# Optimization experiments

Hardware: AMD Instinct MI355X
Metric: run time of the kernel (lower is better)

## Reference

```python
import jax, jax.numpy as jnp
import numpy as np

D, H, KVH, HD = 2048, 16, 8, 128
D1, D2 = 32, 64  # get_decompose_dim(2048)
BITS = 8


def fake_quant(x, bits=BITS):
    # per-row (last-axis) symmetric fake quant with straight-through estimator
    qmax = float(2 ** (bits - 1) - 1)
    s = jnp.maximum(jnp.max(jnp.abs(x), axis=-1, keepdims=True) / qmax, 1e-8)
    q = jnp.clip(jnp.round(x / s), -qmax, qmax) * s
    return x + jax.lax.stop_gradient(q - x)


def rotate_half(x):
    h = x.shape[-1] // 2
    return jnp.concatenate([-x[..., h:], x[..., :h]], axis=-1)


def setup_inputs() -> dict:
    key = jax.random.key(0)
    ks = jax.random.split(key, 10)
    B, S = 1, 2048
    hidden_states = jax.random.normal(ks[0], (B, S, D), jnp.float32)
    # rotary embeddings
    inv_freq = 1.0 / (10000.0 ** (jnp.arange(0, HD, 2, dtype=jnp.float32) / HD))
    t = jnp.arange(S, dtype=jnp.float32)
    freqs = t[:, None] * inv_freq[None, :]
    emb = jnp.concatenate([freqs, freqs], axis=-1)
    cos, sin = jnp.cos(emb)[None], jnp.sin(emb)[None]  # [1,S,HD]
    # projection weights
    Wq = jax.random.normal(ks[1], (H * HD, D), jnp.float32) * 0.02
    Wk = jax.random.normal(ks[2], (KVH * HD, D), jnp.float32) * 0.02
    Wv = jax.random.normal(ks[3], (KVH * HD, D), jnp.float32) * 0.02
    Wo = jax.random.normal(ks[4], (D, H * HD), jnp.float32) * 0.02
    # learned invertible transforms (near-identity for conditioning)
    L = jnp.eye(D1) + 0.02 * jax.random.normal(ks[5], (D1, D1), jnp.float32)
    R = jnp.eye(D2) + 0.02 * jax.random.normal(ks[6], (D2, D2), jnp.float32)
    diag = 1.0 + 0.1 * jax.random.uniform(ks[7], (D,), jnp.float32)
    Tk = jnp.eye(HD) + 0.02 * jax.random.normal(ks[8], (HD, HD), jnp.float32)
    Tv = jnp.eye(HD) + 0.02 * jax.random.normal(ks[9], (HD, HD), jnp.float32)
    return dict(hidden_states=hidden_states, cos=cos, sin=sin, Wq=Wq, Wk=Wk,
                Wv=Wv, Wo=Wo, L=L, R=R, diag=diag, Tk=Tk, Tv=Tv)


def reference(hidden_states, cos, sin, Wq, Wk, Wv, Wo, L, R, diag, Tk, Tv):
    B, S, _ = hidden_states.shape
    groups = H // KVH
    scale = HD ** -0.5
    # ---- ln_trans: x' = (x * diag) @ kron(L, R) ----
    P = diag[:, None] * jnp.kron(L, R)               # [D, D]
    Pinv = jnp.kron(jnp.linalg.inv(L), jnp.linalg.inv(R)) * (1.0 / diag)[None, :]
    x = hidden_states @ P
    x_q = fake_quant(x)                               # per-token activation quant
    # ---- QKV with transform fused into weights (qa_trans), then weight quant ----
    q = x_q @ fake_quant(Wq @ Pinv.T).T               # [B,S,H*HD]
    k = x_q @ fake_quant(Wk @ Pinv.T).T               # [B,S,KVH*HD]
    Wv_eff = jnp.einsum('hd,khD->kdD', Tv, (Wv @ Pinv.T).reshape(KVH, HD, D))
    v = x_q @ fake_quant(Wv_eff.reshape(KVH * HD, D)).T  # v already in Tv space
    # ---- heads + RoPE ----
    q = q.reshape(B, S, H, HD).transpose(0, 2, 1, 3)
    k = k.reshape(B, S, KVH, HD).transpose(0, 2, 1, 3)
    v = v.reshape(B, S, KVH, HD).transpose(0, 2, 1, 3)
    c, s_ = cos[:, None], sin[:, None]                # [1,1,S,HD]
    q = q * c + rotate_half(q) * s_
    k = k * c + rotate_half(k) * s_
    # ---- kcache trans + quant: q @ inv(Tk)^T, k @ Tk (dot product preserved) ----
    q = q @ jnp.linalg.inv(Tk).T
    k = fake_quant(k @ Tk)
    v = fake_quant(v)
    # ---- eager causal attention with GQA ----
    k = jnp.repeat(k, groups, axis=1)
    v = jnp.repeat(v, groups, axis=1)
    scores = jnp.einsum('bhqd,bhkd->bhqk', q, k) * scale
    mask = jnp.tril(jnp.ones((S, S), bool))
    scores = jnp.where(mask, scores, jnp.finfo(scores.dtype).min)
    w = jax.nn.softmax(scores, axis=-1)
    o = jnp.einsum('bhqk,bhkd->bhqd', w, v)
    o = o.transpose(0, 2, 1, 3).reshape(B, S, H * HD)
    # ---- undo vcache trans per head, then quantized o_proj ----
    o = (o.reshape(B, S, H, HD) @ jnp.linalg.inv(Tv)).reshape(B, S, H * HD)
    out = fake_quant(o) @ fake_quant(Wo).T
    return out
```

## Files before the change

kernel.cpp:

```cpp
#include <hip/hip_runtime.h>
#include <math.h>

typedef unsigned short u16;
typedef __attribute__((ext_vector_type(8))) short bf16x8;
typedef __attribute__((ext_vector_type(4))) float f32x4;

__device__ __forceinline__ u16 f2bf(float x) {
    union { float f; unsigned int u; } c; c.f = x;
    unsigned int r = c.u + 0x7fffu + ((c.u >> 16) & 1u);
    return (u16)(r >> 16);
}
__device__ __forceinline__ float bf2f(u16 h) {
    union { unsigned int u; float f; } c; c.u = ((unsigned int)h) << 16;
    return c.f;
}
__device__ __forceinline__ bf16x8 ld16(const u16* p) {
    bf16x8 r;
    ((uint2*)&r)[0] = *(const uint2*)p;
    ((uint2*)&r)[1] = *(const uint2*)(p + 4);
    return r;
}
__device__ __forceinline__ void st8(u16* dst, uint4 r) {
    *(uint2*)dst = make_uint2(r.x, r.y);
    *(uint2*)(dst + 4) = make_uint2(r.z, r.w);
}
__device__ __forceinline__ void cvt8(const float4& v0, const float4& v1,
                                     uint4& hi, uint4& lo) {
    float vv[8] = {v0.x, v0.y, v0.z, v0.w, v1.x, v1.y, v1.z, v1.w};
    u16 h[8], l[8];
#pragma unroll
    for (int e = 0; e < 8; ++e) {
        h[e] = f2bf(vv[e]);
        l[e] = f2bf(vv[e] - bf2f(h[e]));
    }
    hi.x = h[0] | ((unsigned)h[1] << 16); hi.y = h[2] | ((unsigned)h[3] << 16);
    hi.z = h[4] | ((unsigned)h[5] << 16); hi.w = h[6] | ((unsigned)h[7] << 16);
    lo.x = l[0] | ((unsigned)l[1] << 16); lo.y = l[2] | ((unsigned)l[3] << 16);
    lo.z = l[4] | ((unsigned)l[5] << 16); lo.w = l[6] | ((unsigned)l[7] << 16);
}

__global__ __launch_bounds__(1024) void p0_kernel(
    const float* __restrict__ A0, float* __restrict__ I0,
    const float* __restrict__ A1, float* __restrict__ I1,
    const float* __restrict__ A2, float* __restrict__ I2,
    const float* __restrict__ A3, float* __restrict__ I3,
    const float* __restrict__ X, const float* __restrict__ dg,
    const float* __restrict__ Lk, const float* __restrict__ Rk,
    u16* __restrict__ Yq, float* __restrict__ Ysc) {
    const int tid = threadIdx.x;
    if (blockIdx.x < 4) {
        __shared__ float rowbuf[2][128];
        const float* A; float* out; int N;
        switch (blockIdx.x) {
            case 0:  A = A0; out = I0; N = 32;  break;
            case 1:  A = A1; out = I1; N = 64;  break;
            case 2:  A = A2; out = I2; N = 128; break;
            default: A = A3; out = I3; N = 128; break;
        }
        const int i = tid >> 3, g = tid & 7, c0 = g * 16;
        const int rl = (i & 7) << 3;
        float r[16];
#pragma unroll
        for (int e = 0; e < 16; ++e) {
            int j = c0 + e;
            r[e] = (i < N && j < N) ? A[i * N + j] : ((i == j) ? 1.0f : 0.0f);
        }
        if (i == 0) {
            float ip = 1.0f / __shfl(r[0], rl, 64);
#pragma unroll
            for (int e = 0; e < 16; ++e)
                rowbuf[0][c0 + e] = (c0 + e == 0) ? ip : r[e] * ip;
        }
        __syncthreads();
        const int ng = N >> 4;
        for (int k16 = 0; k16 < ng; ++k16) {
#pragma unroll
            for (int e = 0; e < 16; ++e) {
                const int k = (k16 << 4) + e;
                const int pb = k & 1;
                float ci = __shfl(r[e], rl + k16, 64);
                float4 rb0 = *(const float4*)&rowbuf[pb][c0];
                float4 rb1 = *(const float4*)&rowbuf[pb][c0 + 4];
                float4 rb2 = *(const float4*)&rowbuf[pb][c0 + 8];
                float4 rb3 = *(const float4*)&rowbuf[pb][c0 + 12];
                float rb[16] = {rb0.x, rb0.y, rb0.z, rb0.w, rb1.x, rb1.y, rb1.z, rb1.w,
                                rb2.x, rb2.y, rb2.z, rb2.w, rb3.x, rb3.y, rb3.z, rb3.w};
                if (i == k) {
#pragma unroll
                    for (int e2 = 0; e2 < 16; ++e2) r[e2] = rb[e2];
                } else {
#pragma unroll
                    for (int e2 = 0; e2 < 16; ++e2) {
                        float v = (c0 + e2 == k) ? 0.0f : r[e2];
                        r[e2] = fmaf(-ci, rb[e2], v);
                    }
                }
                if (k + 1 < N && i == k + 1) {
                    const int en = (e + 1) & 15;
                    const int gn = (e == 15) ? k16 + 1 : k16;
                    float ip = 1.0f / __shfl(r[en], rl + gn, 64);
#pragma unroll
                    for (int e2 = 0; e2 < 16; ++e2)
                        rowbuf[pb ^ 1][c0 + e2] = (c0 + e2 == k + 1) ? ip : r[e2] * ip;
                }
                __syncthreads();
            }
        }
        if (i < N)
#pragma unroll
            for (int e = 0; e < 16; ++e) {
                int j = c0 + e;
                if (j < N) out[i * N + j] = r[e];
            }
    } else {
        __shared__ float Al[32 * 33];
        __shared__ float Bl[64 * 65];
        __shared__ float Xl[32 * 65];
        __shared__ float Tl[32 * 65];
        __shared__ float red[1024];
        if (tid < 1024) {
            int c = tid >> 5, a = tid & 31;
            Al[c * 33 + a] = Lk[c * 32 + a];
        }
        for (int idx = tid; idx < 4096; idx += 1024) {
            int d = idx >> 6, b = idx & 63;
            Bl[d * 65 + b] = Rk[d * 64 + b];
        }
        const int row = blockIdx.x - 4;
        const float* xp = X + (size_t)row * 2048;
        for (int j = tid; j < 2048; j += 1024)
            Xl[(j >> 6) * 65 + (j & 63)] = xp[j] * dg[j];
        __syncthreads();

        float t2[2], y2[2];
#pragma unroll
        for (int o = 0; o < 2; ++o) {
            int idx = tid * 2 + o;
            int c = idx >> 6, b = idx & 63;
            float acc = 0.0f;
            for (int d = 0; d < 64; ++d)
                acc = fmaf(Xl[c * 65 + d], Bl[d * 65 + b], acc);
            t2[o] = acc;
        }
        {
            int idx0 = tid * 2;
            Tl[(idx0 >> 6) * 65 + (idx0 & 63)] = t2[0];
            Tl[((idx0 + 1) >> 6) * 65 + ((idx0 + 1) & 63)] = t2[1];
        }
        __syncthreads();
#pragma unroll
        for (int o = 0; o < 2; ++o) {
            int idx = tid * 2 + o;
            int a = idx >> 6, b = idx & 63;
            float acc = 0.0f;
            for (int c2 = 0; c2 < 32; ++c2)
                acc = fmaf(Al[c2 * 33 + a], Tl[c2 * 65 + b], acc);
            y2[o] = acc;
        }
        float am = fmaxf(fabsf(y2[0]), fabsf(y2[1]));
        red[tid] = am;
        __syncthreads();
        for (int s = 512; s > 0; s >>= 1) {
            if (tid < s) red[tid] = fmaxf(red[tid], red[tid + s]);
            __syncthreads();
        }
        float scale = fmaxf(red[0] / 127.0f, 1e-8f);
        if (tid == 0) Ysc[row] = scale;
        unsigned pk;
        {
            float v0 = rintf(y2[0] / scale);
            v0 = fminf(fmaxf(v0, -127.0f), 127.0f);
            float v1 = rintf(y2[1] / scale);
            v1 = fminf(fmaxf(v1, -127.0f), 127.0f);
            pk = f2bf(v0) | ((unsigned)f2bf(v1) << 16);
        }
        *(unsigned*)(Yq + (size_t)row * 2048 + tid * 2) = pk;
    }
}

template <int TA, int TB, int OUTQ, int DIV>
__global__ __launch_bounds__(256) void kron_kernel(
    const float* __restrict__ X, const float* __restrict__ scIn,
    const float* __restrict__ A, const float* __restrict__ B,
    u16* __restrict__ Yq, float* __restrict__ Ysc, float* __restrict__ Yf) {
    __shared__ float Al[32 * 33];
    __shared__ float Bl[64 * 65];
    __shared__ float Xl[32 * 65];
    __shared__ float Tl[32 * 65];
    __shared__ float red[256];
    const int tid = threadIdx.x;
    for (int idx = tid; idx < 1024; idx += 256) {
        int c = idx >> 5, a = idx & 31;
        Al[c * 33 + a] = TA ? A[a * 32 + c] : A[c * 32 + a];
    }
    for (int idx = tid; idx < 4096; idx += 256) {
        int d = idx >> 6, b = idx & 63;
        Bl[d * 65 + b] = TB ? B[b * 64 + d] : B[d * 64 + b];
    }
    const int row = blockIdx.x;
    const float* xp = X + (size_t)row * 2048;
    for (int j = tid; j < 2048; j += 256) {
        float sc = DIV ? (1.0f / scIn[j]) : scIn[j];
        Xl[(j >> 6) * 65 + (j & 63)] = xp[j] * sc;
    }
    __syncthreads();

    const int c = tid >> 3, b0 = (tid & 7) * 8;
    float t[8];
#pragma unroll
    for (int jj = 0; jj < 8; ++jj) t[jj] = 0.0f;
    for (int d = 0; d < 64; ++d) {
        float xv = Xl[c * 65 + d];
#pragma unroll
        for (int jj = 0; jj < 8; ++jj)
            t[jj] = fmaf(xv, Bl[d * 65 + b0 + jj], t[jj]);
    }
#pragma unroll
    for (int jj = 0; jj < 8; ++jj) Tl[c * 65 + b0 + jj] = t[jj];
    __syncthreads();

    const int a = tid >> 3;
    float y[8];
#pragma unroll
    for (int jj = 0; jj < 8; ++jj) y[jj] = 0.0f;
    for (int c2 = 0; c2 < 32; ++c2) {
        float av = Al[c2 * 33 + a];
#pragma unroll
        for (int jj = 0; jj < 8; ++jj)
            y[jj] = fmaf(av, Tl[c2 * 65 + b0 + jj], y[jj]);
    }

    if (OUTQ) {
        float am = 0.0f;
#pragma unroll
        for (int jj = 0; jj < 8; ++jj) am = fmaxf(am, fabsf(y[jj]));
        red[tid] = am;
        __syncthreads();
        for (int s = 128; s > 0; s >>= 1) {
            if (tid < s) red[tid] = fmaxf(red[tid], red[tid + s]);
            __syncthreads();
        }
        float scale = fmaxf(red[0] / 127.0f, 1e-8f);
        if (tid == 0) Ysc[row] = scale;
        u16 qq[8];
#pragma unroll
        for (int e = 0; e < 8; ++e) {
            float v = rintf(y[e] / scale);
            v = fminf(fmaxf(v, -127.0f), 127.0f);
            qq[e] = f2bf(v);
        }
        uint4 pk;
        pk.x = qq[0] | ((unsigned)qq[1] << 16); pk.y = qq[2] | ((unsigned)qq[3] << 16);
        pk.z = qq[4] | ((unsigned)qq[5] << 16); pk.w = qq[6] | ((unsigned)qq[7] << 16);
        *(uint4*)(Yq + (size_t)row * 2048 + tid * 8) = pk;
    } else {
        float* yp = Yf + (size_t)row * 2048 + tid * 8;
        *(float4*)yp = make_float4(y[0], y[1], y[2], y[3]);
        *(float4*)(yp + 4) = make_float4(y[4], y[5], y[6], y[7]);
    }
}

__global__ void split_s_kernel(const float* __restrict__ in, int ld, int cols,
                               u16* __restrict__ hi, u16* __restrict__ lo) {
    int idx = (blockIdx.x * 256 + threadIdx.x) * 4;
    int r = idx / cols, c = idx % cols;
    float4 v = *(const float4*)(in + (size_t)r * ld + c);
    ushort4 h, l;
    h.x = f2bf(v.x); l.x = f2bf(v.x - bf2f(h.x));
    h.y = f2bf(v.y); l.y = f2bf(v.y - bf2f(h.y));
    h.z = f2bf(v.z); l.z = f2bf(v.z - bf2f(h.z));
    h.w = f2bf(v.w); l.w = f2bf(v.w - bf2f(h.w));
    *(ushort4*)(hi + idx) = h;
    *(ushort4*)(lo + idx) = l;
}

__global__ void split_t_kernel(const float* __restrict__ in, u16* __restrict__ hi,
                               u16* __restrict__ lo, int rows, int cols) {
    __shared__ float t[32][33];
    int bx = blockIdx.x, by = blockIdx.y;
    int lx = threadIdx.x & 31, ly = threadIdx.x >> 5;
    for (int r = ly; r < 32; r += 8)
        t[r][lx] = in[(size_t)(by * 32 + r) * cols + bx * 32 + lx];
    __syncthreads();
    for (int r = ly; r < 32; r += 8) {
        float v = t[lx][r];
        size_t o = (size_t)(bx * 32 + r) * rows + by * 32 + lx;
        u16 h = f2bf(v);
        hi[o] = h;
        lo[o] = f2bf(v - bf2f(h));
    }
}

__global__ void split_t3_kernel(const float* __restrict__ i0, u16* __restrict__ h0,
                                u16* __restrict__ l0,
                                const float* __restrict__ i1, u16* __restrict__ h1,
                                u16* __restrict__ l1,
                                const float* __restrict__ i2, u16* __restrict__ h2,
                                u16* __restrict__ l2) {
    __shared__ float t[32][33];
    const float* in; u16* hi; u16* lo;
    switch (blockIdx.z) {
        case 0:  in = i0; hi = h0; lo = l0; break;
        case 1:  in = i1; hi = h1; lo = l1; break;
        default: in = i2; hi = h2; lo = l2; break;
    }
    int bx = blockIdx.x, by = blockIdx.y;
    int lx = threadIdx.x & 31, ly = threadIdx.x >> 5;
    for (int r = ly; r < 32; r += 8)
        t[r][lx] = in[(size_t)(by * 32 + r) * 128 + bx * 32 + lx];
    __syncthreads();
    for (int r = ly; r < 32; r += 8) {
        float v = t[lx][r];
        size_t o = (size_t)(bx * 32 + r) * 128 + by * 32 + lx;
        u16 h = f2bf(v);
        hi[o] = h;
        lo[o] = f2bf(v - bf2f(h));
    }
}

__global__ __launch_bounds__(256) void gemm_kernel(
    const u16* __restrict__ Ah, const u16* __restrict__ Al, int lda, long aZ, int aDiv,
    const u16* __restrict__ Bh, const u16* __restrict__ Bl, int ldb, long bZ, int bDiv,
    float* __restrict__ C, int ldc, long cZ, int cDiv, int K, float alpha) {
    const int m0 = blockIdx.y * 128, n0 = blockIdx.x * 128;
    const int z = blockIdx.z;
    {
        long ao = (long)(z >> aDiv) * aZ;
        long bo = (long)(z >> bDiv) * bZ;
        Ah += ao; Al += ao; Bh += bo; Bl += bo;
    }
    __shared__ u16 Ash[2][2][128][36];
    __shared__ u16 Bsh[2][2][128][36];

    const int tid = threadIdx.x, lane = tid & 63, wave = tid >> 6;
    const int wr = wave >> 1, wc = wave & 1;
    const int fr = lane & 15, fg8 = (lane >> 4) * 8;
    const int srow = tid >> 2, cc8 = (tid & 3) * 8;

    f32x4 acc[4][4];
#pragma unroll
    for (int m = 0; m < 4; ++m)
#pragma unroll
        for (int n = 0; n < 4; ++n) acc[m][n] = (f32x4)0.0f;

    uint4 rah0, rah1, ral0, ral1, rbh0, rbh1, rbl0, rbl1;
    const size_t aoff0 = (size_t)(m0 + srow) * lda + cc8;
    const size_t aoff1 = aoff0 + (size_t)64 * lda;
    const size_t boff0 = (size_t)(n0 + srow) * ldb + cc8;
    const size_t boff1 = boff0 + (size_t)64 * ldb;

#define G_LOAD(k0) { \
    rah0 = *(const uint4*)(Ah + aoff0 + (k0)); rah1 = *(const uint4*)(Ah + aoff1 + (k0)); \
    ral0 = *(const uint4*)(Al + aoff0 + (k0)); ral1 = *(const uint4*)(Al + aoff1 + (k0)); \
    rbh0 = *(const uint4*)(Bh + boff0 + (k0)); rbh1 = *(const uint4*)(Bh + boff1 + (k0)); \
    rbl0 = *(const uint4*)(Bl + boff0 + (k0)); rbl1 = *(const uint4*)(Bl + boff1 + (k0)); }
#define G_STORE(b) { \
    st8(&Ash[b][0][srow][cc8], rah0); st8(&Ash[b][0][srow + 64][cc8], rah1); \
    st8(&Ash[b][1][srow][cc8], ral0); st8(&Ash[b][1][srow + 64][cc8], ral1); \
    st8(&Bsh[b][0][srow][cc8], rbh0); st8(&Bsh[b][0][srow + 64][cc8], rbh1); \
    st8(&Bsh[b][1][srow][cc8], rbl0); st8(&Bsh[b][1][srow + 64][cc8], rbl1); }

    const int nk = K >> 5;
    G_LOAD(0);
    G_STORE(0);
    __syncthreads();
    int cur = 0;
    for (int ik = 0; ik < nk; ++ik) {
        if (ik + 1 < nk) G_LOAD((ik + 1) << 5);
        bf16x8 bh[4], bl[4];
#pragma unroll
        for (int n = 0; n < 4; ++n) {
            bh[n] = ld16(&Bsh[cur][0][wc * 64 + n * 16 + fr][fg8]);
            bl[n] = ld16(&Bsh[cur][1][wc * 64 + n * 16 + fr][fg8]);
        }
#pragma unroll
        for (int m = 0; m < 4; ++m) {
            bf16x8 ah = ld16(&Ash[cur][0][wr * 64 + m * 16 + fr][fg8]);
            bf16x8 al = ld16(&Ash[cur][1][wr * 64 + m * 16 + fr][fg8]);
#pragma unroll
            for (int n = 0; n < 4; ++n) {
                acc[m][n] = __builtin_amdgcn_mfma_f32_16x16x32_bf16(ah, bh[n], acc[m][n], 0, 0, 0);
                acc[m][n] = __builtin_amdgcn_mfma_f32_16x16x32_bf16(ah, bl[n], acc[m][n], 0, 0, 0);
                acc[m][n] = __builtin_amdgcn_mfma_f32_16x16x32_bf16(al, bh[n], acc[m][n], 0, 0, 0);
            }
        }
        if (ik + 1 < nk) G_STORE(cur ^ 1);
        __syncthreads();
        cur ^= 1;
    }
    const long co = (long)(z >> cDiv) * cZ;
#pragma unroll
    for (int m = 0; m < 4; ++m) {
        int row_b = m0 + wr * 64 + m * 16 + (fg8 >> 1);
#pragma unroll
        for (int n = 0; n < 4; ++n) {
            int col = n0 + wc * 64 + n * 16 + fr;
#pragma unroll
            for (int j = 0; j < 4; ++j)
                C[co + (long)(row_b + j) * ldc + col] = alpha * acc[m][n][j];
        }
    }
#undef G_LOAD
#undef G_STORE
}

__global__ __launch_bounds__(256) void gemm_af32_kernel(
    const float* __restrict__ A, int lda, long aZ, int aDiv,
    const u16* __restrict__ Bh, const u16* __restrict__ Bl, int ldb, long bZ, int bDiv,
    float* __restrict__ C, int ldc, long cZ, int cDiv, int K, float alpha) {
    const int m0 = blockIdx.y * 128, n0 = blockIdx.x * 128;
    const int z = blockIdx.z;
    A += (long)(z >> aDiv) * aZ;
    {
        long bo = (long)(z >> bDiv) * bZ;
        Bh += bo; Bl += bo;
    }
    __shared__ u16 Ash[2][2][128][36];
    __shared__ u16 Bsh[2][2][128][36];

    const int tid = threadIdx.x, lane = tid & 63, wave = tid >> 6;
    const int wr = wave >> 1, wc = wave & 1;
    const int fr = lane & 15, fg8 = (lane >> 4) * 8;
    const int srow = tid >> 2, cc8 = (tid & 3) * 8;

    f32x4 acc[4][4];
#pragma unroll
    for (int m = 0; m < 4; ++m)
#pragma unroll
        for (int n = 0; n < 4; ++n) acc[m][n] = (f32x4)0.0f;

    float4 a00, a01, a10, a11;
    uint4 rbh0, rbh1, rbl0, rbl1;
    const size_t aoff0 = (size_t)(m0 + srow) * lda + cc8;
    const size_t aoff1 = aoff0 + (size_t)64 * lda;
    const size_t boff0 = (size_t)(n0 + srow) * ldb + cc8;
    const size_t boff1 = boff0 + (size_t)64 * ldb;

#define GA_LOAD(k0) { \
    a00 = *(const float4*)(A + aoff0 + (k0)); a01 = *(const float4*)(A + aoff0 + (k0) + 4); \
    a10 = *(const float4*)(A + aoff1 + (k0)); a11 = *(const float4*)(A + aoff1 + (k0) + 4); \
    rbh0 = *(const uint4*)(Bh + boff0 + (k0)); rbh1 = *(const uint4*)(Bh + boff1 + (k0)); \
    rbl0 = *(const uint4*)(Bl + boff0 + (k0)); rbl1 = *(const uint4*)(Bl + boff1 + (k0)); }
#define GA_STORE(b) { \
    uint4 h0_, l0_, h1_, l1_; \
    cvt8(a00, a01, h0_, l0_); cvt8(a10, a11, h1_, l1_); \
    st8(&Ash[b][0][srow][cc8], h0_); st8(&Ash[b][0][srow + 64][cc8], h1_); \
    st8(&Ash[b][1][srow][cc8], l0_); st8(&Ash[b][1][srow + 64][cc8], l1_); \
    st8(&Bsh[b][0][srow][cc8], rbh0); st8(&Bsh[b][0][srow + 64][cc8], rbh1); \
    st8(&Bsh[b][1][srow][cc8], rbl0); st8(&Bsh[b][1][srow + 64][cc8], rbl1); }

    const int nk = K >> 5;
    GA_LOAD(0);
    GA_STORE(0);
    __syncthreads();
    int cur = 0;
    for (int ik = 0; ik < nk; ++ik) {
        if (ik + 1 < nk) GA_LOAD((ik + 1) << 5);
        bf16x8 bh[4], bl[4];
#pragma unroll
        for (int n = 0; n < 4; ++n) {
            bh[n] = ld16(&Bsh[cur][0][wc * 64 + n * 16 + fr][fg8]);
            bl[n] = ld16(&Bsh[cur][1][wc * 64 + n * 16 + fr][fg8]);
        }
#pragma unroll
        for (int m = 0; m < 4; ++m) {
            bf16x8 ah = ld16(&Ash[cur][0][wr * 64 + m * 16 + fr][fg8]);
            bf16x8 al = ld16(&Ash[cur][1][wr * 64 + m * 16 + fr][fg8]);
#pragma unroll
            for (int n = 0; n < 4; ++n) {
                acc[m][n] = __builtin_amdgcn_mfma_f32_16x16x32_bf16(ah, bh[n], acc[m][n], 0, 0, 0);
                acc[m][n] = __builtin_amdgcn_mfma_f32_16x16x32_bf16(ah, bl[n], acc[m][n], 0, 0, 0);
                acc[m][n] = __builtin_amdgcn_mfma_f32_16x16x32_bf16(al, bh[n], acc[m][n], 0, 0, 0);
            }
        }
        if (ik + 1 < nk) GA_STORE(cur ^ 1);
        __syncthreads();
        cur ^= 1;
    }
    const long co = (long)(z >> cDiv) * cZ;
#pragma unroll
    for (int m = 0; m < 4; ++m) {
        int row_b = m0 + wr * 64 + m * 16 + (fg8 >> 1);
#pragma unroll
        for (int n = 0; n < 4; ++n) {
            int col = n0 + wc * 64 + n * 16 + fr;
#pragma unroll
            for (int j = 0; j < 4; ++j)
                C[co + (long)(row_b + j) * ldc + col] = alpha * acc[m][n][j];
        }
    }
#undef GA_LOAD
#undef GA_STORE
}

__global__ __launch_bounds__(256) void gemm_int_kernel(
    const u16* __restrict__ A, int lda, const float* __restrict__ sa,
    const u16* __restrict__ B, int ldb, const float* __restrict__ sb,
    float* __restrict__ C, int ldc, long aZ, long bZ, long cZ, int K) {
    const int m0 = blockIdx.y * 128, n0 = blockIdx.x * 128;
    const int z = blockIdx.z;
    A += (long)z * aZ; B += (long)z * bZ; C += (long)z * cZ;
    __shared__ u16 Ash[2][128][36];
    __shared__ u16 Bsh[2][128][36];
    const int tid = threadIdx.x, lane = tid & 63, wave = tid >> 6;
    const int wr = wave >> 1, wc = wave & 1;
    const int fr = lane & 15, fg8 = (lane >> 4) * 8;
    const int srow = tid >> 2, cc8 = (tid & 3) * 8;
    f32x4 acc[4][4];
#pragma unroll
    for (int m = 0; m < 4; ++m)
#pragma unroll
        for (int n = 0; n < 4; ++n) acc[m][n] = (f32x4)0.0f;

    uint4 ra0, ra1, rb0, rb1;
    const size_t aoff0 = (size_t)(m0 + srow) * lda + cc8;
    const size_t aoff1 = aoff0 + (size_t)64 * lda;
    const size_t boff0 = (size_t)(n0 + srow) * ldb + cc8;
    const size_t boff1 = boff0 + (size_t)64 * ldb;
#define GI_LOAD(k0) { \
    ra0 = *(const uint4*)(A + aoff0 + (k0)); ra1 = *(const uint4*)(A + aoff1 + (k0)); \
    rb0 = *(const uint4*)(B + boff0 + (k0)); rb1 = *(const uint4*)(B + boff1 + (k0)); }
#define GI_STORE(b) { \
    st8(&Ash[b][srow][cc8], ra0); st8(&Ash[b][srow + 64][cc8], ra1); \
    st8(&Bsh[b][srow][cc8], rb0); st8(&Bsh[b][srow + 64][cc8], rb1); }
    const int nk = K >> 5;
    GI_LOAD(0);
    GI_STORE(0);
    __syncthreads();
    int cur = 0;
    for (int ik = 0; ik < nk; ++ik) {
        if (ik + 1 < nk) GI_LOAD((ik + 1) << 5);
        bf16x8 bfr[4];
#pragma unroll
        for (int n = 0; n < 4; ++n)
            bfr[n] = ld16(&Bsh[cur][wc * 64 + n * 16 + fr][fg8]);
#pragma unroll
        for (int m = 0; m < 4; ++m) {
            bf16x8 ah = ld16(&Ash[cur][wr * 64 + m * 16 + fr][fg8]);
#pragma unroll
            for (int n = 0; n < 4; ++n)
                acc[m][n] = __builtin_amdgcn_mfma_f32_16x16x32_bf16(ah, bfr[n], acc[m][n], 0, 0, 0);
        }
        if (ik + 1 < nk) GI_STORE(cur ^ 1);
        __syncthreads();
        cur ^= 1;
    }
#pragma unroll
    for (int m = 0; m < 4; ++m) {
        int row_b = m0 + wr * 64 + m * 16 + (fg8 >> 1);
#pragma unroll
        for (int n = 0; n < 4; ++n) {
            int col = n0 + wc * 64 + n * 16 + fr;
            float sc = sb[col];
#pragma unroll
            for (int j = 0; j < 4; ++j)
                C[(long)(row_b + j) * ldc + col] = acc[m][n][j] * sa[row_b + j] * sc;
        }
    }
#undef GI_LOAD
#undef GI_STORE
}

__global__ void rowquant_int_kernel(const float* __restrict__ x, u16* __restrict__ qi,
                                    float* __restrict__ sc, int cols) {
    __shared__ float red[256];
    int row = blockIdx.x, tid = threadIdx.x;
    const float* p = x + (size_t)row * cols;
    u16* q = qi + (size_t)row * cols;
    float m = 0.0f;
    for (int j = tid; j < cols; j += 256) m = fmaxf(m, fabsf(p[j]));
    red[tid] = m; __syncthreads();
    for (int s = 128; s > 0; s >>= 1) {
        if (tid < s) red[tid] = fmaxf(red[tid], red[tid + s]);
        __syncthreads();
    }
    float scale = fmaxf(red[0] / 127.0f, 1e-8f);
    if (tid == 0) sc[row] = scale;
    for (int j = tid; j < cols; j += 256) {
        float v = rintf(p[j] / scale);
        v = fminf(fmaxf(v, -127.0f), 127.0f);
        q[j] = f2bf(v);
    }
}

__global__ void rowquant_w_kernel(const float* __restrict__ x, u16* __restrict__ qi,
                                  float* __restrict__ sc) {
    int row = blockIdx.x * 4 + (threadIdx.x >> 6);
    int lane = threadIdx.x & 63;
    const float* p = x + (size_t)row * 128;
    float2 v = *(const float2*)(p + lane * 2);
    float m = fmaxf(fabsf(v.x), fabsf(v.y));
#pragma unroll
    for (int off = 1; off < 64; off <<= 1) m = fmaxf(m, __shfl_xor(m, off));
    float scale = fmaxf(m / 127.0f, 1e-8f);
    if (lane == 0) sc[row] = scale;
    float a = rintf(v.x / scale), b = rintf(v.y / scale);
    a = fminf(fmaxf(a, -127.0f), 127.0f);
    b = fminf(fmaxf(b, -127.0f), 127.0f);
    unsigned pk = f2bf(a) | ((unsigned)f2bf(b) << 16);
    *(unsigned*)(qi + (size_t)row * 128 + lane * 2) = pk;
}

__global__ __launch_bounds__(256) void quantT_v_kernel(
    const float* __restrict__ QKVf, u16* __restrict__ vTi, float* __restrict__ vs) {
    __shared__ u16 tile[128][72];
    const int st = blockIdx.x, g = blockIdx.y;
    const int t = threadIdx.x;
    const int sl = t >> 2, dc = (t & 3) * 32;
    const int s = st * 64 + sl;
    const float* p = QKVf + (size_t)s * 4096 + 3072 + g * 128 + dc;
    float4 vr[8];
    float m = 0.0f;
#pragma unroll
    for (int q = 0; q < 8; ++q) {
        vr[q] = *(const float4*)(p + q * 4);
        m = fmaxf(m, fmaxf(fmaxf(fabsf(vr[q].x), fabsf(vr[q].y)),
                           fmaxf(fabsf(vr[q].z), fabsf(vr[q].w))));
    }
    m = fmaxf(m, __shfl_xor(m, 1));
    m = fmaxf(m, __shfl_xor(m, 2));
    float scale = fmaxf(m / 127.0f, 1e-8f);
    if ((t & 3) == 0) vs[s * 8 + g] = scale;
#pragma unroll
    for (int q = 0; q < 8; ++q) {
        float vv[4] = {vr[q].x, vr[q].y, vr[q].z, vr[q].w};
#pragma unroll
        for (int e = 0; e < 4; ++e) {
            float qv = rintf(vv[e] / scale);
            qv = fminf(fmaxf(qv, -127.0f), 127.0f);
            tile[dc + q * 4 + e][sl] = f2bf(qv);
        }
    }
    __syncthreads();
    const int d = t >> 1, sc0 = (t & 1) * 32;
    u16* dst = vTi + (size_t)(g * 128 + d) * 2048 + st * 64 + sc0;
#pragma unroll
    for (int q = 0; q < 4; ++q) {
        u16 tmp[8];
#pragma unroll
        for (int e = 0; e < 8; ++e) tmp[e] = tile[d][sc0 + q * 8 + e];
        uint4 v;
        v.x = tmp[0] | ((unsigned)tmp[1] << 16); v.y = tmp[2] | ((unsigned)tmp[3] << 16);
        v.z = tmp[4] | ((unsigned)tmp[5] << 16); v.w = tmp[6] | ((unsigned)tmp[7] << 16);
        *(uint4*)(dst + q * 8) = v;
    }
}

__global__ void rope_kernel(float* __restrict__ x, int ld, int cb,
                            const float* __restrict__ c, const float* __restrict__ s,
                            int nh) {
    int idx = blockIdx.x * 256 + threadIdx.x;
    int d = idx & 63;
    int t = idx >> 6;
    int h = t % nh;
    int sq = t / nh;
    size_t base = (size_t)sq * ld + cb + h * 128;
    float a = x[base + d], b = x[base + d + 64];
    float c1 = c[sq * 128 + d], s1 = s[sq * 128 + d];
    float c2 = c[sq * 128 + d + 64], s2 = s[sq * 128 + d + 64];
    x[base + d] = a * c1 - b * s1;
    x[base + d + 64] = b * c2 + a * s2;
}

__global__ __launch_bounds__(256, 2) void flash_kernel(
    const float* __restrict__ q2f,
    const u16* __restrict__ k2i, const float* __restrict__ ksc,
    const u16* __restrict__ vTi, const float* __restrict__ vsc,
    float* __restrict__ obuf, float* __restrict__ mlbuf) {
    const int h = blockIdx.x, part = blockIdx.y, qt = 31 - blockIdx.z, g = h >> 1;
    __shared__ u16 Ksh[2][64 * 128];
    __shared__ u16 Vsh[2][128 * 64];
    __shared__ u16 Psh[4][16 * 64];
    __shared__ float Kss[2][64];
    __shared__ float Vss[2][64];

    const int tid = threadIdx.x, lane = tid & 63, w = tid >> 6;
    const int lc = lane & 15, lg = lane >> 4;
    const float scale = 0.08838834764831845f;
    const float LOG2E = 1.4426950408889634f;
    const float THR = 10.0f;

    bf16x8 qh[4], ql[4];
    {
        int s = qt * 64 + w * 16 + lc;
        const float* qp = q2f + (size_t)s * 2048 + h * 128 + lg * 8;
#pragma unroll
        for (int kk = 0; kk < 4; ++kk) {
            float4 v0 = *(const float4*)(qp + kk * 32);
            float4 v1 = *(const float4*)(qp + kk * 32 + 4);
            float vv[8] = {v0.x, v0.y, v0.z, v0.w, v1.x, v1.y, v1.z, v1.w};
#pragma unroll
            for (int e = 0; e < 8; ++e) {
                float x = vv[e] * scale;
                u16 hh = f2bf(x);
                qh[kk][e] = (short)hh;
                ql[kk][e] = (short)f2bf(x - bf2f(hh));
            }
        }
    }

    f32x4 acc_o[8];
#pragma unroll
    for (int nn = 0; nn < 8; ++nn) acc_o[nn] = (f32x4)0.0f;
    float mj = -1e30f, lj = 0.0f;

    const int p0cnt = (qt + 2) >> 1;
    const int tn = (part == 0) ? p0cnt : (qt + 1 - p0cnt);
    const int t0 = (part == 0) ? 0 : p0cnt;

    const int kr = tid >> 2, kc = tid & 3;
    const int vd = tid >> 1, vc0 = (tid & 1) * 4;
    uint4 kg0, kg1, kg2, kg3, vg0, vg1, vg2, vg3;
    float sreg = 0.0f;

#define STAGE_LOAD(tg) { \
    const int j0_ = (tg) * 64; \
    const u16* kp_ = k2i + (size_t)(j0_ + kr) * 1024 + g * 128; \
    kg0 = *(const uint4*)(kp_ + kc * 8); \
    kg1 = *(const uint4*)(kp_ + (kc + 4) * 8); \
    kg2 = *(const uint4*)(kp_ + (kc + 8) * 8); \
    kg3 = *(const uint4*)(kp_ + (kc + 12) * 8); \
    const u16* vp_ = vTi + (size_t)(g * 128 + vd) * 2048 + j0_; \
    vg0 = *(const uint4*)(vp_ + vc0 * 8); \
    vg1 = *(const uint4*)(vp_ + (vc0 + 1) * 8); \
    vg2 = *(const uint4*)(vp_ + (vc0 + 2) * 8); \
    vg3 = *(const uint4*)(vp_ + (vc0 + 3) * 8); \
    if (tid < 64) sreg = ksc[(j0_ + tid) * 8 + g] * LOG2E; \
    else if (tid < 128) sreg = vsc[(j0_ + tid - 64) * 8 + g]; }

#define STAGE_WRITE(b) { \
    *(uint4*)(&Ksh[b][kr * 128 + ((kc ^ (kr & 7)) << 3)]) = kg0; \
    *(uint4*)(&Ksh[b][kr * 128 + (((kc + 4) ^ (kr & 7)) << 3)]) = kg1; \
    *(uint4*)(&Ksh[b][kr * 128 + (((kc + 8) ^ (kr & 7)) << 3)]) = kg2; \
    *(uint4*)(&Ksh[b][kr * 128 + (((kc + 12) ^ (kr & 7)) << 3)]) = kg3; \
    *(uint4*)(&Vsh[b][vd * 64 + ((vc0 ^ (vd & 7)) << 3)]) = vg0; \
    *(uint4*)(&Vsh[b][vd * 64 + (((vc0 + 1) ^ (vd & 7)) << 3)]) = vg1; \
    *(uint4*)(&Vsh[b][vd * 64 + (((vc0 + 2) ^ (vd & 7)) << 3)]) = vg2; \
    *(uint4*)(&Vsh[b][vd * 64 + (((vc0 + 3) ^ (vd & 7)) << 3)]) = vg3; \
    if (tid < 64) Kss[b][tid] = sreg; \
    else if (tid < 128) Vss[b][tid - 64] = sreg; }

    if (tn > 0) {
        STAGE_LOAD(t0);
        STAGE_WRITE(0);
    }
    __syncthreads();
    for (int t = 0; t < tn; ++t) {
        const int cur = t & 1;
        const int tg = t0 + t;
        if (t + 1 < tn) STAGE_LOAD(t0 + t + 1);

        f32x4 accs[4];
#pragma unroll
        for (int n = 0; n < 4; ++n) accs[n] = (f32x4)0.0f;
#pragma unroll
        for (int n = 0; n < 4; ++n) {
#pragma unroll
            for (int kk = 0; kk < 4; ++kk) {
                bf16x8 kf = ld16(&Ksh[cur][(n * 16 + lc) * 128 + (((kk * 4 + lg) ^ (lc & 7)) << 3)]);
                accs[n] = __builtin_amdgcn_mfma_f32_16x16x32_bf16(kf, qh[kk], accs[n], 0, 0, 0);
                accs[n] = __builtin_amdgcn_mfma_f32_16x16x32_bf16(kf, ql[kk], accs[n], 0, 0, 0);
            }
        }
#pragma unroll
        for (int n = 0; n < 4; ++n)
#pragma unroll
            for (int j = 0; j < 4; ++j)
                accs[n][j] *= Kss[cur][n * 16 + lg * 4 + j];
        if (tg == qt) {
            int qg = qt * 64 + w * 16 + lc;
#pragma unroll
            for (int n = 0; n < 4; ++n)
#pragma unroll
                for (int j = 0; j < 4; ++j) {
                    int kgl = tg * 64 + n * 16 + lg * 4 + j;
                    if (kgl > qg) accs[n][j] = -3.0e38f;
                }
        }

        float pm = accs[0][0];
#pragma unroll
        for (int n = 0; n < 4; ++n)
#pragma unroll
            for (int j = 0; j < 4; ++j) pm = fmaxf(pm, accs[n][j]);
        pm = fmaxf(pm, __shfl_xor(pm, 16));
        pm = fmaxf(pm, __shfl_xor(pm, 32));
        bool need = pm > mj + THR;
        float mn = need ? pm : mj;
        float sf = need ? exp2f(mj - mn) : 1.0f;
        mj = mn;
        if (__any(need)) {
            float sfj[4];
#pragma unroll
            for (int j = 0; j < 4; ++j) sfj[j] = __shfl(sf, lg * 4 + j);
#pragma unroll
            for (int nn = 0; nn < 8; ++nn)
#pragma unroll
                for (int j = 0; j < 4; ++j) acc_o[nn][j] *= sfj[j];
        }
        float rowsum = 0.0f;
#pragma unroll
        for (int n = 0; n < 4; ++n)
#pragma unroll
            for (int j = 0; j < 4; ++j) {
                float p = exp2f(accs[n][j] - mj);
                accs[n][j] = p;
                rowsum += p;
            }
        rowsum += __shfl_xor(rowsum, 16);
        rowsum += __shfl_xor(rowsum, 32);
        lj = lj * sf + rowsum;

#pragma unroll
        for (int n = 0; n < 4; ++n)
#pragma unroll
            for (int jp = 0; jp < 2; ++jp) {
                int k = n * 16 + lg * 4 + jp * 2;
                unsigned val = f2bf(accs[n][jp * 2] * Vss[cur][k]) |
                               ((unsigned)f2bf(accs[n][jp * 2 + 1] * Vss[cur][k + 1]) << 16);
                int cch = k >> 3;
                *(unsigned*)(&Psh[w][lc * 64 + ((cch ^ (lc & 7)) << 3) + (k & 7)]) = val;
            }
        bf16x8 pf[2];
#pragma unroll
        for (int kk = 0; kk < 2; ++kk)
            pf[kk] = ld16(&Psh[w][lc * 64 + (((kk * 4 + lg) ^ (lc & 7)) << 3)]);

#pragma unroll
        for (int nn = 0; nn < 8; ++nn) {
            int d = nn * 16 + lc;
#pragma unroll
            for (int kk = 0; kk < 2; ++kk) {
                bf16x8 vf = ld16(&Vsh[cur][d * 64 + (((kk * 4 + lg) ^ (d & 7)) << 3)]);
                acc_o[nn] = __builtin_amdgcn_mfma_f32_16x16x32_bf16(pf[kk], vf, acc_o[nn], 0, 0, 0);
            }
        }
        if (t + 1 < tn) STAGE_WRITE(cur ^ 1);
        __syncthreads();
    }
#undef STAGE_LOAD
#undef STAGE_WRITE

    float* op = obuf + (size_t)part * 4194304 + ((size_t)h * 2048 + qt * 64 + w * 16) * 128;
#pragma unroll
    for (int nn = 0; nn < 8; ++nn)
#pragma unroll
        for (int j = 0; j < 4; ++j)
            op[(lg * 4 + j) * 128 + nn * 16 + lc] = acc_o[nn][j];
    if (lg == 0) {
        int rs = h * 2048 + qt * 64 + w * 16 + lc;
        mlbuf[part * 65536 + rs] = mj;
        mlbuf[part * 65536 + 32768 + rs] = lj;
    }
}

__global__ void combine_kernel(const float* __restrict__ o01,
                               const float* __restrict__ ml,
                               float* __restrict__ of) {
    int idx = blockIdx.x * 256 + threadIdx.x;
    int hs = idx >> 7;
    float m0 = ml[hs], l0 = ml[32768 + hs];
    float m1 = ml[65536 + hs], l1 = ml[98304 + hs];
    float m = fmaxf(m0, m1);
    float w0 = exp2f(m0 - m), w1 = exp2f(m1 - m);
    float l = l0 * w0 + l1 * w1;
    of[idx] = (o01[idx] * w0 + o01[4194304 + idx] * w1) / l;
}

__global__ void add2_kernel(const float* __restrict__ a, const float* __restrict__ b,
                            float* __restrict__ o) {
    int i = (blockIdx.x * 256 + threadIdx.x) * 4;
    float4 x = *(const float4*)(a + i);
    float4 y = *(const float4*)(b + i);
    x.x += y.x; x.y += y.y; x.z += y.z; x.w += y.w;
    *(float4*)(o + i) = x;
}

extern "C" void kernel_launch(void* const* d_in, const int* in_sizes, int n_in,
                              void* d_out, int out_size, void* d_ws, size_t ws_size,
                              hipStream_t stream) {
    const float* hidden = (const float*)d_in[0];
    const float* cosp   = (const float*)d_in[1];
    const float* sinp   = (const float*)d_in[2];
    const float* Wq     = (const float*)d_in[3];
    const float* Wk     = (const float*)d_in[4];
    const float* Wv     = (const float*)d_in[5];
    const float* Wo     = (const float*)d_in[6];
    const float* Lp     = (const float*)d_in[7];
    const float* Rp     = (const float*)d_in[8];
    const float* diag   = (const float*)d_in[9];
    const float* Tkp    = (const float*)d_in[10];
    const float* Tvp    = (const float*)d_in[11];
    float* out = (float*)d_out;

    const size_t MiB = 1ull << 20;
    char* W = (char*)d_ws;
    auto F = [&](size_t mb) { return (float*)(W + mb * MiB); };
    auto U = [&](size_t mb) { return (u16*)(W + mb * MiB); };
    const long HP2 = 2097152;

    float* dsc   = (float*)d_out;
    float* invL  = dsc;
    float* invR  = dsc + 1024;
    float* invTk = dsc + 5120;
    float* invTv = dsc + 21504;
    u16* sm = (u16*)(dsc + 37888);
    u16* invTk_sh = sm;              u16* invTk_sl = sm + 16384;
    u16* TkT_sh   = sm + 2 * 16384;  u16* TkT_sl   = sm + 3 * 16384;
    u16* invTvT_sh= sm + 4 * 16384;  u16* invTvT_sl= sm + 5 * 16384;
    u16* TvT_sh   = sm + 6 * 16384;  u16* TvT_sl   = sm + 7 * 16384;

    float* xs    = F(88);
    float* wqkvs = xs + 2048;
    float* wqs   = wqkvs;
    float* wks   = wqkvs + 2048;
    float* wvs   = wqkvs + 3072;
    float* k2s   = wqkvs + 4096;
    float* vs    = k2s + 16384;
    float* o2s   = vs + 16384;
    float* wos   = o2s + 2048;

    u16* Xi = U(0);
    p0_kernel<<<2052, 1024, 0, stream>>>(Lp, invL, Rp, invR, Tkp, invTk, Tvp, invTv,
                                         hidden, diag, Lp, Rp, Xi, xs);
    split_s_kernel<<<16, 256, 0, stream>>>(invTk, 128, 128, invTk_sh, invTk_sl);
    split_t3_kernel<<<dim3(4, 4, 3), 256, 0, stream>>>(
        Tkp, TkT_sh, TkT_sl, invTv, invTvT_sh, invTvT_sl, Tvp, TvT_sh, TvT_sl);

    u16* WQKVi = U(8);
    u16* WVi   = U(20);
    float* WvP = F(24);
    kron_kernel<1, 1, 1, 1><<<2048, 256, 0, stream>>>(Wq, diag, invL, invR, WQKVi, wqs, 0);
    kron_kernel<1, 1, 1, 1><<<1024, 256, 0, stream>>>(Wk, diag, invL, invR, U(16), wks, 0);
    kron_kernel<1, 1, 0, 1><<<1024, 256, 0, stream>>>(Wv, diag, invL, invR, 0, 0, WvP);

    u16* WVPt_s = U(32);
    split_t_kernel<<<dim3(64, 32), 256, 0, stream>>>(WvP, WVPt_s, WVPt_s + HP2, 1024, 2048);
    float* WVf = F(72);
    gemm_kernel<<<dim3(16, 1, 8), 256, 0, stream>>>(
        TvT_sh, TvT_sl, 128, 0, 0, WVPt_s, WVPt_s + HP2, 1024, 128, 0,
        WVf, 2048, (long)128 * 2048, 0, 128, 1.0f);
    rowquant_int_kernel<<<1024, 256, 0, stream>>>(WVf, WVi, wvs, 2048);

    float* QKVf = F(40);
    gemm_int_kernel<<<dim3(32, 16), 256, 0, stream>>>(Xi, 2048, xs, WQKVi, 2048, wqkvs,
                                                      QKVf, 4096, 0, 0, 0, 2048);

    rope_kernel<<<8192, 256, 0, stream>>>(QKVf, 4096, 0, cosp, sinp, 16);
    rope_kernel<<<4096, 256, 0, stream>>>(QKVf, 4096, 2048, cosp, sinp, 8);

    float* k2f = F(32);
    gemm_af32_kernel<<<dim3(1, 16, 8), 256, 0, stream>>>(
        QKVf + 2048, 4096, 128, 0, TkT_sh, TkT_sl, 128, 0, 0,
        k2f, 1024, 128, 0, 128, 1.0f);
    u16* k2i = U(8);
    rowquant_w_kernel<<<4096, 256, 0, stream>>>(k2f, k2i, k2s);

    u16* vTi = U(16);
    quantT_v_kernel<<<dim3(32, 8), 256, 0, stream>>>(QKVf, vTi, vs);

    float* q2f = F(72);
    gemm_af32_kernel<<<dim3(1, 16, 16), 256, 0, stream>>>(
        QKVf, 4096, 128, 0, invTk_sh, invTk_sl, 128, 0, 0,
        q2f, 2048, 128, 0, 128, 1.0f);

    float* o01 = F(40);
    float* ml  = F(32);
    flash_kernel<<<dim3(16, 2, 32), 256, 0, stream>>>(q2f, k2i, k2s, vTi, vs, o01, ml);
    float* of = F(0);
    combine_kernel<<<16384, 256, 0, stream>>>(o01, ml, of);

    float* o2f = F(16);
    gemm_af32_kernel<<<dim3(1, 16, 16), 256, 0, stream>>>(
        of, 128, 262144, 0, invTvT_sh, invTvT_sl, 128, 0, 0,
        o2f, 2048, 128, 0, 128, 1.0f);
    u16* o2i = U(32);
    rowquant_int_kernel<<<2048, 256, 0, stream>>>(o2f, o2i, o2s, 2048);
    u16* Woi = U(40);
    rowquant_int_kernel<<<2048, 256, 0, stream>>>(Wo, Woi, wos, 2048);
    float* C0 = F(48);
    gemm_int_kernel<<<dim3(16, 16, 2), 256, 0, stream>>>(o2i, 2048, o2s, Woi, 2048, wos,
                                                         C0, 2048, 1024, 1024, 4194304, 1024);
    add2_kernel<<<4096, 256, 0, stream>>>(C0, C0 + 4194304, out);

    (void)in_sizes; (void)n_in; (void)out_size; (void)ws_size;
}
```

Before: 459.5 us.

## Fuse Q/K transform GEMMs, fold split-attention combine into o-transform GEMM

Merges the separate K and Q head-transform GEMM launches into one grid that picks its operands by z index. It also folds the two-partition flash-attention combine (max/sum rescale) into the A-operand load of the inverse-Tv GEMM, which removes the combine kernel and its intermediate buffer. The two row-quant launches for o2 and Wo are merged into one launch. Together these cut launch count and one full read/write of the attention output, at the cost of hardcoded specialised kernels.

```diff
diff --git a/kernel.cpp b/kernel.cpp
--- a/kernel.cpp
+++ b/kernel.cpp
@@ -118,7 +118,7 @@
         __shared__ float Xl[32 * 65];
         __shared__ float Tl[32 * 65];
         __shared__ float red[1024];
-        if (tid < 1024) {
+        {
             int c = tid >> 5, a = tid & 31;
             Al[c * 33 + a] = Lk[c * 32 + a];
         }
@@ -404,20 +404,23 @@
 #undef G_STORE
 }
 
-__global__ __launch_bounds__(256) void gemm_af32_kernel(
-    const float* __restrict__ A, int lda, long aZ, int aDiv,
-    const u16* __restrict__ Bh, const u16* __restrict__ Bl, int ldb, long bZ, int bDiv,
-    float* __restrict__ C, int ldc, long cZ, int cDiv, int K, float alpha) {
-    const int m0 = blockIdx.y * 128, n0 = blockIdx.x * 128;
+__global__ __launch_bounds__(256) void gemm_qk_kernel(
+    const float* __restrict__ QKVf,
+    const u16* __restrict__ iTk_h, const u16* __restrict__ iTk_l,
+    const u16* __restrict__ TkT_h, const u16* __restrict__ TkT_l,
+    float* __restrict__ q2f, float* __restrict__ k2f) {
+    const int m0 = blockIdx.y * 128;
     const int z = blockIdx.z;
-    A += (long)(z >> aDiv) * aZ;
-    {
-        long bo = (long)(z >> bDiv) * bZ;
-        Bh += bo; Bl += bo;
-    }
+    const bool isQ = (z < 16);
+    const float* A = QKVf + (isQ ? z * 128 : 2048 + (z - 16) * 128);
+    const u16* Bh = isQ ? iTk_h : TkT_h;
+    const u16* Bl = isQ ? iTk_l : TkT_l;
+    float* C = isQ ? (q2f + z * 128) : (k2f + (z - 16) * 128);
+    const int ldc = isQ ? 2048 : 1024;
+    const int lda = 4096, ldb = 128, K = 128;
+
     __shared__ u16 Ash[2][2][128][36];
     __shared__ u16 Bsh[2][2][128][36];
-
     const int tid = threadIdx.x, lane = tid & 63, wave = tid >> 6;
     const int wr = wave >> 1, wc = wave & 1;
     const int fr = lane & 15, fg8 = (lane >> 4) * 8;
@@ -433,15 +436,15 @@
     uint4 rbh0, rbh1, rbl0, rbl1;
     const size_t aoff0 = (size_t)(m0 + srow) * lda + cc8;
     const size_t aoff1 = aoff0 + (size_t)64 * lda;
-    const size_t boff0 = (size_t)(n0 + srow) * ldb + cc8;
+    const size_t boff0 = (size_t)srow * ldb + cc8;
     const size_t boff1 = boff0 + (size_t)64 * ldb;
 
-#define GA_LOAD(k0) { \
+#define GQ_LOAD(k0) { \
     a00 = *(const float4*)(A + aoff0 + (k0)); a01 = *(const float4*)(A + aoff0 + (k0) + 4); \
     a10 = *(const float4*)(A + aoff1 + (k0)); a11 = *(const float4*)(A + aoff1 + (k0) + 4); \
     rbh0 = *(const uint4*)(Bh + boff0 + (k0)); rbh1 = *(const uint4*)(Bh + boff1 + (k0)); \
     rbl0 = *(const uint4*)(Bl + boff0 + (k0)); rbl1 = *(const uint4*)(Bl + boff1 + (k0)); }
-#define GA_STORE(b) { \
+#define GQ_STORE(b) { \
     uint4 h0_, l0_, h1_, l1_; \
     cvt8(a00, a01, h0_, l0_); cvt8(a10, a11, h1_, l1_); \
     st8(&Ash[b][0][srow][cc8], h0_); st8(&Ash[b][0][srow + 64][cc8], h1_); \
@@ -450,12 +453,12 @@
     st8(&Bsh[b][1][srow][cc8], rbl0); st8(&Bsh[b][1][srow + 64][cc8], rbl1); }
 
     const int nk = K >> 5;
-    GA_LOAD(0);
-    GA_STORE(0);
+    GQ_LOAD(0);
+    GQ_STORE(0);
     __syncthreads();
     int cur = 0;
     for (int ik = 0; ik < nk; ++ik) {
-        if (ik + 1 < nk) GA_LOAD((ik + 1) << 5);
+        if (ik + 1 < nk) GQ_LOAD((ik + 1) << 5);
         bf16x8 bh[4], bl[4];
 #pragma unroll
         for (int n = 0; n < 4; ++n) {
@@ -473,24 +476,134 @@
                 acc[m][n] = __builtin_amdgcn_mfma_f32_16x16x32_bf16(al, bh[n], acc[m][n], 0, 0, 0);
             }
         }
-        if (ik + 1 < nk) GA_STORE(cur ^ 1);
+        if (ik + 1 < nk) GQ_STORE(cur ^ 1);
         __syncthreads();
         cur ^= 1;
     }
-    const long co = (long)(z >> cDiv) * cZ;
 #pragma unroll
     for (int m = 0; m < 4; ++m) {
         int row_b = m0 + wr * 64 + m * 16 + (fg8 >> 1);
 #pragma unroll
         for (int n = 0; n < 4; ++n) {
-            int col = n0 + wc * 64 + n * 16 + fr;
+            int col = wc * 64 + n * 16 + fr;
 #pragma unroll
             for (int j = 0; j < 4; ++j)
-                C[co + (long)(row_b + j) * ldc + col] = alpha * acc[m][n][j];
-        }
-    }
-#undef GA_LOAD
-#undef GA_STORE
+                C[(long)(row_b + j) * ldc + col] = acc[m][n][j];
+        }
+    }
+#undef GQ_LOAD
+#undef GQ_STORE
+}
+
+__global__ __launch_bounds__(256) void gemm_o2_kernel(
+    const float* __restrict__ o01, const float* __restrict__ ml,
+    const u16* __restrict__ Bh, const u16* __restrict__ Bl,
+    float* __restrict__ C) {
+    const int m0 = blockIdx.y * 128;
+    const int z = blockIdx.z;
+    const int ldb = 128, K = 128, ldc = 2048;
+    __shared__ u16 Ash[2][2][128][36];
+    __shared__ u16 Bsh[2][2][128][36];
+    const int tid = threadIdx.x, lane = tid & 63, wave = tid >> 6;
+    const int wr = wave >> 1, wc = wave & 1;
+    const int fr = lane & 15, fg8 = (lane >> 4) * 8;
+    const int srow = tid >> 2, cc8 = (tid & 3) * 8;
+
+    f32x4 acc[4][4];
+#pragma unroll
+    for (int m = 0; m < 4; ++m)
+#pragma unroll
+        for (int n = 0; n < 4; ++n) acc[m][n] = (f32x4)0.0f;
+
+    const int rs0 = z * 2048 + m0 + srow;
+    const int rs1 = rs0 + 64;
+    float w0a, w1a, w0b, w1b;
+    {
+        float ma0 = ml[rs0], la0 = ml[32768 + rs0];
+        float ma1 = ml[65536 + rs0], la1 = ml[98304 + rs0];
+        float mm = fmaxf(ma0, ma1);
+        float e0 = exp2f(ma0 - mm), e1 = exp2f(ma1 - mm);
+        float linv = 1.0f / (la0 * e0 + la1 * e1);
+        w0a = e0 * linv; w1a = e1 * linv;
+        float mb0 = ml[rs1], lb0 = ml[32768 + rs1];
+        float mb1 = ml[65536 + rs1], lb1 = ml[98304 + rs1];
+        float mmb = fmaxf(mb0, mb1);
+        float f0 = exp2f(mb0 - mmb), f1 = exp2f(mb1 - mmb);
+        float linvb = 1.0f / (lb0 * f0 + lb1 * f1);
+        w0b = f0 * linvb; w1b = f1 * linvb;
+    }
+    const float* A0 = o01 + (size_t)rs0 * 128 + cc8;
+    const float* A1 = o01 + 4194304 + (size_t)rs0 * 128 + cc8;
+    const float* B0 = o01 + (size_t)rs1 * 128 + cc8;
+    const float* B1 = o01 + 4194304 + (size_t)rs1 * 128 + cc8;
+
+    float4 a00, a01, a10, a11;
+    uint4 rbh0, rbh1, rbl0, rbl1;
+    const size_t boff0 = (size_t)srow * ldb + cc8;
+    const size_t boff1 = boff0 + (size_t)64 * ldb;
+
+#define CMB4(p, q, w0_, w1_) make_float4( \
+    (p).x * (w0_) + (q).x * (w1_), (p).y * (w0_) + (q).y * (w1_), \
+    (p).z * (w0_) + (q).z * (w1_), (p).w * (w0_) + (q).w * (w1_))
+#define GO_LOAD(k0) { \
+    float4 p0 = *(const float4*)(A0 + (k0)), p1 = *(const float4*)(A1 + (k0)); \
+    float4 p2 = *(const float4*)(A0 + (k0) + 4), p3 = *(const float4*)(A1 + (k0) + 4); \
+    a00 = CMB4(p0, p1, w0a, w1a); a01 = CMB4(p2, p3, w0a, w1a); \
+    float4 q0 = *(const float4*)(B0 + (k0)), q1 = *(const float4*)(B1 + (k0)); \
+    float4 q2 = *(const float4*)(B0 + (k0) + 4), q3 = *(const float4*)(B1 + (k0) + 4); \
+    a10 = CMB4(q0, q1, w0b, w1b); a11 = CMB4(q2, q3, w0b, w1b); \
+    rbh0 = *(const uint4*)(Bh + boff0 + (k0)); rbh1 = *(const uint4*)(Bh + boff1 + (k0)); \
+    rbl0 = *(const uint4*)(Bl + boff0 + (k0)); rbl1 = *(const uint4*)(Bl + boff1 + (k0)); }
+#define GO_STORE(b) { \
+    uint4 h0_, l0_, h1_, l1_; \
+    cvt8(a00, a01, h0_, l0_); cvt8(a10, a11, h1_, l1_); \
+    st8(&Ash[b][0][srow][cc8], h0_); st8(&Ash[b][0][srow + 64][cc8], h1_); \
+    st8(&Ash[b][1][srow][cc8], l0_); st8(&Ash[b][1][srow + 64][cc8], l1_); \
+    st8(&Bsh[b][0][srow][cc8], rbh0); st8(&Bsh[b][0][srow + 64][cc8], rbh1); \
+    st8(&Bsh[b][1][srow][cc8], rbl0); st8(&Bsh[b][1][srow + 64][cc8], rbl1); }
+
+    const int nk = K >> 5;
+    GO_LOAD(0);
+    GO_STORE(0);
+    __syncthreads();
+    int cur = 0;
+    for (int ik = 0; ik < nk; ++ik) {
+        if (ik + 1 < nk) GO_LOAD((ik + 1) << 5);
+        bf16x8 bh[4], bl[4];
+#pragma unroll
+        for (int n = 0; n < 4; ++n) {
+            bh[n] = ld16(&Bsh[cur][0][wc * 64 + n * 16 + fr][fg8]);
+            bl[n] = ld16(&Bsh[cur][1][wc * 64 + n * 16 + fr][fg8]);
+        }
+#pragma unroll
+        for (int m = 0; m < 4; ++m) {
+            bf16x8 ah = ld16(&Ash[cur][0][wr * 64 + m * 16 + fr][fg8]);
+            bf16x8 al = ld16(&Ash[cur][1][wr * 64 + m * 16 + fr][fg8]);
+#pragma unroll
+            for (int n = 0; n < 4; ++n) {
+                acc[m][n] = __builtin_amdgcn_mfma_f32_16x16x32_bf16(ah, bh[n], acc[m][n], 0, 0, 0);
+                acc[m][n] = __builtin_amdgcn_mfma_f32_16x16x32_bf16(ah, bl[n], acc[m][n], 0, 0, 0);
+                acc[m][n] = __builtin_amdgcn_mfma_f32_16x16x32_bf16(al, bh[n], acc[m][n], 0, 0, 0);
+            }
+        }
+        if (ik + 1 < nk) GO_STORE(cur ^ 1);
+        __syncthreads();
+        cur ^= 1;
+    }
+#pragma unroll
+    for (int m = 0; m < 4; ++m) {
+        int row_b = m0 + wr * 64 + m * 16 + (fg8 >> 1);
+#pragma unroll
+        for (int n = 0; n < 4; ++n) {
+            int col = wc * 64 + n * 16 + fr;
+#pragma unroll
+            for (int j = 0; j < 4; ++j)
+                C[(long)(row_b + j) * ldc + z * 128 + col] = acc[m][n][j];
+        }
+    }
+#undef GO_LOAD
+#undef GO_STORE
+#undef CMB4
 }
 
 __global__ __launch_bounds__(256) void gemm_int_kernel(
@@ -583,6 +696,33 @@
     }
 }
 
+__global__ void rowquant2_kernel(const float* __restrict__ x0, u16* __restrict__ q0,
+                                 float* __restrict__ s0,
+                                 const float* __restrict__ x1, u16* __restrict__ q1,
+                                 float* __restrict__ s1) {
+    __shared__ float red[256];
+    int bid = blockIdx.x, tid = threadIdx.x;
+    const float* p; u16* q; float* sc; int row;
+    if (bid < 2048) { p = x0; q = q0; sc = s0; row = bid; }
+    else            { p = x1; q = q1; sc = s1; row = bid - 2048; }
+    p += (size_t)row * 2048;
+    q += (size_t)row * 2048;
+    float m = 0.0f;
+    for (int j = tid; j < 2048; j += 256) m = fmaxf(m, fabsf(p[j]));
+    red[tid] = m; __syncthreads();
+    for (int s = 128; s > 0; s >>= 1) {
+        if (tid < s) red[tid] = fmaxf(red[tid], red[tid + s]);
+        __syncthreads();
+    }
+    float scale = fmaxf(red[0] / 127.0f, 1e-8f);
+    if (tid == 0) sc[row] = scale;
+    for (int j = tid; j < 2048; j += 256) {
+        float v = rintf(p[j] / scale);
+        v = fminf(fmaxf(v, -127.0f), 127.0f);
+        q[j] = f2bf(v);
+    }
+}
+
 __global__ void rowquant_w_kernel(const float* __restrict__ x, u16* __restrict__ qi,
                                   float* __restrict__ sc) {
     int row = blockIdx.x * 4 + (threadIdx.x >> 6);
@@ -662,6 +802,15 @@
     x[base + d + 64] = b * c2 + a * s2;
 }
 
+__global__ void add2_kernel(const float* __restrict__ a, const float* __restrict__ b,
+                            float* __restrict__ o) {
+    int i = (blockIdx.x * 256 + threadIdx.x) * 4;
+    float4 x = *(const float4*)(a + i);
+    float4 y = *(const float4*)(b + i);
+    x.x += y.x; x.y += y.y; x.z += y.z; x.w += y.w;
+    *(float4*)(o + i) = x;
+}
+
 __global__ __launch_bounds__(256, 2) void flash_kernel(
     const float* __restrict__ q2f,
     const u16* __restrict__ k2i, const float* __restrict__ ksc,
@@ -852,28 +1001,6 @@
         mlbuf[part * 65536 + rs] = mj;
         mlbuf[part * 65536 + 32768 + rs] = lj;
     }
-}
-
-__global__ void combine_kernel(const float* __restrict__ o01,
-                               const float* __restrict__ ml,
-                               float* __restrict__ of) {
-    int idx = blockIdx.x * 256 + threadIdx.x;
-    int hs = idx >> 7;
-    float m0 = ml[hs], l0 = ml[32768 + hs];
-    float m1 = ml[65536 + hs], l1 = ml[98304 + hs];
-    float m = fmaxf(m0, m1);
-    float w0 = exp2f(m0 - m), w1 = exp2f(m1 - m);
-    float l = l0 * w0 + l1 * w1;
-    of[idx] = (o01[idx] * w0 + o01[4194304 + idx] * w1) / l;
-}
-
-__global__ void add2_kernel(const float* __restrict__ a, const float* __restrict__ b,
-                            float* __restrict__ o) {
-    int i = (blockIdx.x * 256 + threadIdx.x) * 4;
-    float4 x = *(const float4*)(a + i);
-    float4 y = *(const float4*)(b + i);
-    x.x += y.x; x.y += y.y; x.z += y.z; x.w += y.w;
-    *(float4*)(o + i) = x;
 }
 
 extern "C" void kernel_launch(void* const* d_in, const int* in_sizes, int n_in,
@@ -949,35 +1076,26 @@
     rope_kernel<<<8192, 256, 0, stream>>>(QKVf, 4096, 0, cosp, sinp, 16);
     rope_kernel<<<4096, 256, 0, stream>>>(QKVf, 4096, 2048, cosp, sinp, 8);
 
+    float* q2f = F(72);
     float* k2f = F(32);
-    gemm_af32_kernel<<<dim3(1, 16, 8), 256, 0, stream>>>(
-        QKVf + 2048, 4096, 128, 0, TkT_sh, TkT_sl, 128, 0, 0,
-        k2f, 1024, 128, 0, 128, 1.0f);
+    gemm_qk_kernel<<<dim3(1, 16, 24), 256, 0, stream>>>(
+        QKVf, invTk_sh, invTk_sl, TkT_sh, TkT_sl, q2f, k2f);
     u16* k2i = U(8);
     rowquant_w_kernel<<<4096, 256, 0, stream>>>(k2f, k2i, k2s);
 
     u16* vTi = U(16);
     quantT_v_kernel<<<dim3(32, 8), 256, 0, stream>>>(QKVf, vTi, vs);
-
-    float* q2f = F(72);
-    gemm_af32_kernel<<<dim3(1, 16, 16), 256, 0, stream>>>(
-        QKVf, 4096, 128, 0, invTk_sh, invTk_sl, 128, 0, 0,
-        q2f, 2048, 128, 0, 128, 1.0f);
 
     float* o01 = F(40);
     float* ml  = F(32);
     flash_kernel<<<dim3(16, 2, 32), 256, 0, stream>>>(q2f, k2i, k2s, vTi, vs, o01, ml);
-    float* of = F(0);
-    combine_kernel<<<16384, 256, 0, stream>>>(o01, ml, of);
 
     float* o2f = F(16);
-    gemm_af32_kernel<<<dim3(1, 16, 16), 256, 0, stream>>>(
-        of, 128, 262144, 0, invTvT_sh, invTvT_sl, 128, 0, 0,
-        o2f, 2048, 128, 0, 128, 1.0f);
+    gemm_o2_kernel<<<dim3(1, 16, 16), 256, 0, stream>>>(
+        o01, ml, invTvT_sh, invTvT_sl, o2f);
     u16* o2i = U(32);
-    rowquant_int_kernel<<<2048, 256, 0, stream>>>(o2f, o2i, o2s, 2048);
     u16* Woi = U(40);
-    rowquant_int_kernel<<<2048, 256, 0, stream>>>(Wo, Woi, wos, 2048);
+    rowquant2_kernel<<<4096, 256, 0, stream>>>(o2f, o2i, o2s, Wo, Woi, wos);
     float* C0 = F(48);
     gemm_int_kernel<<<dim3(16, 16, 2), 256, 0, stream>>>(o2i, 2048, o2s, Woi, 2048, wos,
                                                          C0, 2048, 1024, 1024, 4194304, 1024);
```

Result: no change. 454.1 us (-1.2%).
